# Performance work log

Hardware: AMD Instinct MI355X
Metric: run time of the kernel (lower is better)

## Reference

```python
import jax, jax.numpy as jnp
import numpy as np


def setup_inputs() -> dict:
    key = jax.random.key(0)
    k1, k2 = jax.random.split(key)
    B, S, D, E = 4, 4096, 2048, 64
    x = jax.random.normal(k1, (B, S, D), dtype=jnp.float32)
    # nn.Linear default init ~ U(-1/sqrt(D), 1/sqrt(D)); scale down for stability
    w_gate = jax.random.normal(k2, (E, D), dtype=jnp.float32) * (1.0 / np.sqrt(D))
    expert_bias = jnp.zeros((E,), dtype=jnp.float32)
    return {"x": x, "w_gate": w_gate, "expert_bias": expert_bias}


def reference(x, w_gate, expert_bias):
    # gate_logits: [B, S, E]
    gate_logits = jnp.einsum('bsd,ed->bse', x, w_gate)
    gate_weights = jax.nn.sigmoid(gate_logits)
    biased_logits = gate_logits + expert_bias
    k = 8  # num_experts_per_tok
    _, topk_indices = jax.lax.top_k(biased_logits, k)  # [B, S, k]
    topk_weights = jnp.take_along_axis(gate_weights, topk_indices, axis=-1)
    topk_weights = topk_weights / jnp.sum(topk_weights, axis=-1, keepdims=True)
    return topk_weights, topk_indices
```

## Files before the change

kernel.cpp:

```cpp
#include <hip/hip_runtime.h>
#include <math.h>

#define BLOCK 256
#define RB 32
#define BD 64
#define NE 64
#define DDIM 2048
#define TOPK 8
#define NCHUNK (DDIM / BD)

typedef float __attribute__((ext_vector_type(4))) f32x4;

__global__ __launch_bounds__(BLOCK, 2) void gate_kernel(
    const float* __restrict__ x,
    const float* __restrict__ w,
    const float* __restrict__ bias,
    float* __restrict__ out_w,
    float* __restrict__ out_i)
{
    __shared__ float xs[2][RB * BD];
    __shared__ float ws[2][NE * BD];

    const int t    = threadIdx.x;
    const int lane = t & 63;
    const int wid  = t >> 6;
    const int kc   = lane & 15;
    const int kh   = lane >> 4;
    const int row0 = blockIdx.x * RB;

    float acc[8][16];
#pragma unroll
    for (int r = 0; r < 8; ++r)
#pragma unroll
        for (int j = 0; j < 16; ++j) acc[r][j] = 0.f;

#define ISSUE(c_, xb_, wb_)                                                    \
    {                                                                          \
        const int d0_ = (c_) * BD;                                             \
        _Pragma("unroll")                                                      \
        for (int i = 0; i < 2; ++i) {                                          \
            int s  = wid * 2 + i;                                              \
            int f  = s * 256 + lane * 4;                                       \
            int xr = f >> 6, xc = f & 63;                                      \
            __builtin_amdgcn_global_load_lds(                                  \
                (const __attribute__((address_space(1))) unsigned int*)        \
                    (x + (size_t)(row0 + xr) * DDIM + d0_ + xc),               \
                (__attribute__((address_space(3))) unsigned int*)((xb_) + s * 256), \
                16, 0, 0);                                                     \
        }                                                                      \
        _Pragma("unroll")                                                      \
        for (int i = 0; i < 4; ++i) {                                          \
            int s  = wid * 4 + i;                                              \
            int f  = s * 256 + lane * 4;                                       \
            int wr = f >> 6, wc = f & 63;                                      \
            __builtin_amdgcn_global_load_lds(                                  \
                (const __attribute__((address_space(1))) unsigned int*)        \
                    (w + (size_t)wr * DDIM + d0_ + wc),                        \
                (__attribute__((address_space(3))) unsigned int*)((wb_) + s * 256), \
                16, 0, 0);                                                     \
        }                                                                      \
    }

    ISSUE(0, xs[0], ws[0]);

    for (int c = 0; c < NCHUNK; ++c) {
        __syncthreads();

        const float* xsb = xs[c & 1];
        const float* wsb = ws[c & 1];
        if (c + 1 < NCHUNK) ISSUE(c + 1, xs[(c + 1) & 1], ws[(c + 1) & 1]);

        f32x4 xv[8];
#pragma unroll
        for (int r = 0; r < 8; ++r)
            xv[r] = *(const f32x4*)&xsb[(wid * 8 + r) * BD + kc * 4];

#pragma unroll
        for (int j = 0; j < 16; ++j) {
            f32x4 wj = *(const f32x4*)&wsb[(kh * 16 + j) * BD + kc * 4];
#pragma unroll
            for (int r = 0; r < 8; ++r) {
                acc[r][j] += xv[r].x * wj.x;
                acc[r][j] += xv[r].y * wj.y;
                acc[r][j] += xv[r].z * wj.z;
                acc[r][j] += xv[r].w * wj.w;
            }
        }
    }

    const float bias_l = bias[lane];

#pragma unroll
    for (int r = 0; r < 8; ++r) {
        const int gr = row0 + wid * 8 + r;

        float v[16];
#pragma unroll
        for (int j = 0; j < 16; ++j) v[j] = acc[r][j];
#pragma unroll
        for (int o = 8; o; o >>= 1) {
            bool hi = (kc & o) != 0;
#pragma unroll
            for (int j = 0; j < o; ++j) {
                float send = hi ? v[j] : v[j + o];
                float keep = hi ? v[j + o] : v[j];
                v[j] = keep + __shfl_xor(send, o);
            }
        }
        float raw = v[0];
        float sig = 1.f / (1.f + expf(-raw));
        float vv  = raw + bias_l;

        float wsum = 0.f, myw = 0.f;
        int   myidx = 0;
#pragma unroll
        for (int k = 0; k < TOPK; ++k) {
            float m = vv;
#pragma unroll
            for (int off = 32; off; off >>= 1)
                m = fmaxf(m, __shfl_xor(m, off));
            unsigned long long b = __ballot(vv == m);
            int idx = (int)__builtin_ctzll(b);
            float wk = __shfl(sig, idx);
            wsum += wk;
            if (lane == k)  { myw = wk; myidx = idx; }
            if (lane == idx) vv = -INFINITY;
        }
        if (lane < TOPK) {
            out_w[(size_t)gr * TOPK + lane] = myw / wsum;
            out_i[(size_t)gr * TOPK + lane] = (float)myidx;
        }
    }
}

extern "C" void kernel_launch(void* const* d_in, const int* in_sizes, int n_in,
                              void* d_out, int out_size, void* d_ws, size_t ws_size,
                              hipStream_t stream) {
    const float* x    = (const float*)d_in[0];
    const float* w    = (const float*)d_in[1];
    const float* bias = (const float*)d_in[2];
    const int NR = in_sizes[0] / DDIM;
    float* out   = (float*)d_out;
    float* out_w = out;
    float* out_i = out + (size_t)NR * TOPK;

    dim3 grid(NR / RB), block(BLOCK);
    hipLaunchKernelGGL(gate_kernel, grid, block, 0, stream,
                       x, w, bias, out_w, out_i);
}
```

Baseline: 80.06 us.

## Load x tiles directly into registers with double buffering instead of LDS

The x rows are no longer staged through shared memory. Each thread loads its own f32x4 slices of x straight from global memory into two ping-pong register sets, prefetching the next chunk while computing the current one. Only the gate weights still go through the LDS double buffer. This cuts LDS traffic and footprint for x, at the cost of more live registers (16 extra vectors) and loads that are less coalesced, since each wave reads 8 rows with 16 lanes per row. This could raise register pressure under the launch bound of 2.

Measured after the change: 207.4 us. 2.59x slower.

```diff
diff --git a/kernel.cpp b/kernel.cpp
--- a/kernel.cpp
+++ b/kernel.cpp
@@ -18,7 +18,6 @@
     float* __restrict__ out_w,
     float* __restrict__ out_i)
 {
-    __shared__ float xs[2][RB * BD];
     __shared__ float ws[2][NE * BD];
 
     const int t    = threadIdx.x;
@@ -34,20 +33,9 @@
 #pragma unroll
         for (int j = 0; j < 16; ++j) acc[r][j] = 0.f;
 
-#define ISSUE(c_, xb_, wb_)                                                    \
+#define ISSUE_W(c_, wb_)                                                       \
     {                                                                          \
         const int d0_ = (c_) * BD;                                             \
-        _Pragma("unroll")                                                      \
-        for (int i = 0; i < 2; ++i) {                                          \
-            int s  = wid * 2 + i;                                              \
-            int f  = s * 256 + lane * 4;                                       \
-            int xr = f >> 6, xc = f & 63;                                      \
-            __builtin_amdgcn_global_load_lds(                                  \
-                (const __attribute__((address_space(1))) unsigned int*)        \
-                    (x + (size_t)(row0 + xr) * DDIM + d0_ + xc),               \
-                (__attribute__((address_space(3))) unsigned int*)((xb_) + s * 256), \
-                16, 0, 0);                                                     \
-        }                                                                      \
         _Pragma("unroll")                                                      \
         for (int i = 0; i < 4; ++i) {                                          \
             int s  = wid * 4 + i;                                              \
@@ -61,31 +49,42 @@
         }                                                                      \
     }
 
-    ISSUE(0, xs[0], ws[0]);
+    const float* xb = x + (size_t)(row0 + wid * 8) * DDIM + kc * 4;
+#define LOAD_X(dst_, c_)                                                       \
+    {                                                                          \
+        _Pragma("unroll")                                                      \
+        for (int r = 0; r < 8; ++r)                                            \
+            dst_[r] = *(const f32x4*)(xb + (size_t)r * DDIM + (c_) * BD);      \
+    }
 
-    for (int c = 0; c < NCHUNK; ++c) {
-        __syncthreads();
+    f32x4 xA[8], xB[8];
+    LOAD_X(xA, 0);
+    ISSUE_W(0, ws[0]);
 
-        const float* xsb = xs[c & 1];
-        const float* wsb = ws[c & 1];
-        if (c + 1 < NCHUNK) ISSUE(c + 1, xs[(c + 1) & 1], ws[(c + 1) & 1]);
+#define CHUNK_BODY(XCUR, XNXT, c_)                                             \
+    {                                                                          \
+        __syncthreads();     \
+        if ((c_) + 1 < NCHUNK) {                                               \
+            ISSUE_W((c_) + 1, ws[((c_) + 1) & 1]);  \
+            LOAD_X(XNXT, (c_) + 1);                  \
+        }                                                                      \
+        const float* wsb = ws[(c_) & 1];                                       \
+        _Pragma("unroll")                                                      \
+        for (int j = 0; j < 16; ++j) {                                         \
+            f32x4 wj = *(const f32x4*)&wsb[(kh * 16 + j) * BD + kc * 4];       \
+            _Pragma("unroll")                                                  \
+            for (int r = 0; r < 8; ++r) {                                      \
+                acc[r][j] += XCUR[r].x * wj.x;                                 \
+                acc[r][j] += XCUR[r].y * wj.y;                                 \
+                acc[r][j] += XCUR[r].z * wj.z;                                 \
+                acc[r][j] += XCUR[r].w * wj.w;                                 \
+            }                                                                  \
+        }                                                                      \
+    }
 
-        f32x4 xv[8];
-#pragma unroll
-        for (int r = 0; r < 8; ++r)
-            xv[r] = *(const f32x4*)&xsb[(wid * 8 + r) * BD + kc * 4];
-
-#pragma unroll
-        for (int j = 0; j < 16; ++j) {
-            f32x4 wj = *(const f32x4*)&wsb[(kh * 16 + j) * BD + kc * 4];
-#pragma unroll
-            for (int r = 0; r < 8; ++r) {
-                acc[r][j] += xv[r].x * wj.x;
-                acc[r][j] += xv[r].y * wj.y;
-                acc[r][j] += xv[r].z * wj.z;
-                acc[r][j] += xv[r].w * wj.w;
-            }
-        }
+    for (int c = 0; c < NCHUNK; c += 2) {
+        CHUNK_BODY(xA, xB, c);
+        CHUNK_BODY(xB, xA, c + 1);
     }
 
     const float bias_l = bias[lane];
```

## Halve row tile, load x straight to registers, split experts across waves

Applied to the files above, without the earlier changes.

Shrinks the row tile from 32 to 16 and asks for 4 blocks per CU instead of 2. The x tile is no longer staged through LDS: each thread loads its x fragment from global memory directly into registers, prefetching the next chunk after the compute. Waves now split experts into two halves, which halves the accumulator registers, and per-row logits go through a shared buffer before the top-k stage. This aims at higher occupancy and less LDS traffic, at the cost of uncoalesced-ish direct global loads for x and an extra barrier plus LDS round trip.

After: 130.0 us. +62.4%, slower.

```diff
diff --git a/kernel.cpp b/kernel.cpp
--- a/kernel.cpp
+++ b/kernel.cpp
@@ -2,7 +2,7 @@
 #include <math.h>
 
 #define BLOCK 256
-#define RB 32
+#define RB 16
 #define BD 64
 #define NE 64
 #define DDIM 2048
@@ -11,43 +11,34 @@
 
 typedef float __attribute__((ext_vector_type(4))) f32x4;
 
-__global__ __launch_bounds__(BLOCK, 2) void gate_kernel(
+__global__ __launch_bounds__(BLOCK, 4) void gate_kernel(
     const float* __restrict__ x,
     const float* __restrict__ w,
     const float* __restrict__ bias,
     float* __restrict__ out_w,
     float* __restrict__ out_i)
 {
-    __shared__ float xs[2][RB * BD];
     __shared__ float ws[2][NE * BD];
+    __shared__ float logits[RB][NE + 1];
 
     const int t    = threadIdx.x;
     const int lane = t & 63;
     const int wid  = t >> 6;
+    const int rw   = wid & 1;
+    const int eh   = wid >> 1;
     const int kc   = lane & 15;
-    const int kh   = lane >> 4;
+    const int kh   = (lane >> 4) & 3;
     const int row0 = blockIdx.x * RB;
 
-    float acc[8][16];
+    float acc[8][8];
 #pragma unroll
     for (int r = 0; r < 8; ++r)
 #pragma unroll
-        for (int j = 0; j < 16; ++j) acc[r][j] = 0.f;
+        for (int j = 0; j < 8; ++j) acc[r][j] = 0.f;
 
-#define ISSUE(c_, xb_, wb_)                                                    \
+#define ISSUE_W(c_, wb_)                                                       \
     {                                                                          \
         const int d0_ = (c_) * BD;                                             \
-        _Pragma("unroll")                                                      \
-        for (int i = 0; i < 2; ++i) {                                          \
-            int s  = wid * 2 + i;                                              \
-            int f  = s * 256 + lane * 4;                                       \
-            int xr = f >> 6, xc = f & 63;                                      \
-            __builtin_amdgcn_global_load_lds(                                  \
-                (const __attribute__((address_space(1))) unsigned int*)        \
-                    (x + (size_t)(row0 + xr) * DDIM + d0_ + xc),               \
-                (__attribute__((address_space(3))) unsigned int*)((xb_) + s * 256), \
-                16, 0, 0);                                                     \
-        }                                                                      \
         _Pragma("unroll")                                                      \
         for (int i = 0; i < 4; ++i) {                                          \
             int s  = wid * 4 + i;                                              \
@@ -61,23 +52,29 @@
         }                                                                      \
     }
 
-    ISSUE(0, xs[0], ws[0]);
+    const float* xb = x + (size_t)(row0 + rw * 8) * DDIM + kc * 4;
+    f32x4 xv[8];
+#define LOAD_XV(c_)                                                            \
+    {                                                                          \
+        _Pragma("unroll")                                                      \
+        for (int r = 0; r < 8; ++r)                                            \
+            xv[r] = *(const f32x4*)(xb + (size_t)r * DDIM + (c_) * BD);        \
+    }
+
+    ISSUE_W(0, ws[0]);
+    LOAD_XV(0);
+
+    const int wofs = (eh * 32 + kh * 8) * BD + kc * 4;
 
     for (int c = 0; c < NCHUNK; ++c) {
         __syncthreads();
 
-        const float* xsb = xs[c & 1];
+        if (c + 1 < NCHUNK) ISSUE_W(c + 1, ws[(c + 1) & 1]);
+
         const float* wsb = ws[c & 1];
-        if (c + 1 < NCHUNK) ISSUE(c + 1, xs[(c + 1) & 1], ws[(c + 1) & 1]);
-
-        f32x4 xv[8];
 #pragma unroll
-        for (int r = 0; r < 8; ++r)
-            xv[r] = *(const f32x4*)&xsb[(wid * 8 + r) * BD + kc * 4];
-
-#pragma unroll
-        for (int j = 0; j < 16; ++j) {
-            f32x4 wj = *(const f32x4*)&wsb[(kh * 16 + j) * BD + kc * 4];
+        for (int j = 0; j < 8; ++j) {
+            f32x4 wj = *(const f32x4*)&wsb[wofs + j * BD];
 #pragma unroll
             for (int r = 0; r < 8; ++r) {
                 acc[r][j] += xv[r].x * wj.x;
@@ -86,19 +83,20 @@
                 acc[r][j] += xv[r].w * wj.w;
             }
         }
+
+        __builtin_amdgcn_sched_barrier(0);
+        if (c + 1 < NCHUNK) LOAD_XV(c + 1);
     }
-
-    const float bias_l = bias[lane];
 
 #pragma unroll
     for (int r = 0; r < 8; ++r) {
-        const int gr = row0 + wid * 8 + r;
-
-        float v[16];
+        float v[8];
 #pragma unroll
-        for (int j = 0; j < 16; ++j) v[j] = acc[r][j];
+        for (int j = 0; j < 8; ++j) v[j] = acc[r][j];
 #pragma unroll
-        for (int o = 8; o; o >>= 1) {
+        for (int j = 0; j < 8; ++j) v[j] += __shfl_xor(v[j], 8);
+#pragma unroll
+        for (int o = 4; o; o >>= 1) {
             bool hi = (kc & o) != 0;
 #pragma unroll
             for (int j = 0; j < o; ++j) {
@@ -107,7 +105,16 @@
                 v[j] = keep + __shfl_xor(send, o);
             }
         }
-        float raw = v[0];
+        if (kc < 8)
+            logits[rw * 8 + r][eh * 32 + kh * 8 + kc] = v[0];
+    }
+    __syncthreads();
+
+    const float bias_l = bias[lane];
+    for (int rr = 0; rr < 4; ++rr) {
+        const int r  = wid * 4 + rr;
+        const int gr = row0 + r;
+        float raw = logits[r][lane];
         float sig = 1.f / (1.f + expf(-raw));
         float vv  = raw + bias_l;
 
```

## Replace LDS double-buffered staging with direct global-to-register loads

Applied to the files above, without the earlier changes.

Removes the shared-memory staging of x and w tiles (async global_load_lds with double buffering and per-chunk barriers) and has each thread load its x rows and w rows directly from global memory into registers every chunk. This drops LDS traffic and __syncthreads, but it also drops the explicit prefetch overlap. The four warps now each fetch the w tile separately, relying on L1/L2 to absorb the duplication. Holding 24 extra float4 values per thread raises register pressure alongside the 128 accumulators, which may limit occupancy or cause spills.

After: 144.7 us. +80.8%, slower.

```diff
diff --git a/kernel.cpp b/kernel.cpp
--- a/kernel.cpp
+++ b/kernel.cpp
@@ -18,9 +18,6 @@
     float* __restrict__ out_w,
     float* __restrict__ out_i)
 {
-    __shared__ float xs[2][RB * BD];
-    __shared__ float ws[2][NE * BD];
-
     const int t    = threadIdx.x;
     const int lane = t & 63;
     const int wid  = t >> 6;
@@ -34,56 +31,30 @@
 #pragma unroll
         for (int j = 0; j < 16; ++j) acc[r][j] = 0.f;
 
-#define ISSUE(c_, xb_, wb_)                                                    \
-    {                                                                          \
-        const int d0_ = (c_) * BD;                                             \
-        _Pragma("unroll")                                                      \
-        for (int i = 0; i < 2; ++i) {                                          \
-            int s  = wid * 2 + i;                                              \
-            int f  = s * 256 + lane * 4;                                       \
-            int xr = f >> 6, xc = f & 63;                                      \
-            __builtin_amdgcn_global_load_lds(                                  \
-                (const __attribute__((address_space(1))) unsigned int*)        \
-                    (x + (size_t)(row0 + xr) * DDIM + d0_ + xc),               \
-                (__attribute__((address_space(3))) unsigned int*)((xb_) + s * 256), \
-                16, 0, 0);                                                     \
-        }                                                                      \
-        _Pragma("unroll")                                                      \
-        for (int i = 0; i < 4; ++i) {                                          \
-            int s  = wid * 4 + i;                                              \
-            int f  = s * 256 + lane * 4;                                       \
-            int wr = f >> 6, wc = f & 63;                                      \
-            __builtin_amdgcn_global_load_lds(                                  \
-                (const __attribute__((address_space(1))) unsigned int*)        \
-                    (w + (size_t)wr * DDIM + d0_ + wc),                        \
-                (__attribute__((address_space(3))) unsigned int*)((wb_) + s * 256), \
-                16, 0, 0);                                                     \
-        }                                                                      \
-    }
-
-    ISSUE(0, xs[0], ws[0]);
+    const float* xb = x + (size_t)(row0 + wid * 8) * DDIM + kc * 4;
+    const float* wb = w + (size_t)(kh * 16) * DDIM + kc * 4;
 
     for (int c = 0; c < NCHUNK; ++c) {
-        __syncthreads();
-
-        const float* xsb = xs[c & 1];
-        const float* wsb = ws[c & 1];
-        if (c + 1 < NCHUNK) ISSUE(c + 1, xs[(c + 1) & 1], ws[(c + 1) & 1]);
+        const int d0 = c * BD;
 
         f32x4 xv[8];
 #pragma unroll
         for (int r = 0; r < 8; ++r)
-            xv[r] = *(const f32x4*)&xsb[(wid * 8 + r) * BD + kc * 4];
+            xv[r] = *(const f32x4*)(xb + (size_t)r * DDIM + d0);
+
+        f32x4 wv[16];
+#pragma unroll
+        for (int j = 0; j < 16; ++j)
+            wv[j] = *(const f32x4*)(wb + (size_t)j * DDIM + d0);
 
 #pragma unroll
         for (int j = 0; j < 16; ++j) {
-            f32x4 wj = *(const f32x4*)&wsb[(kh * 16 + j) * BD + kc * 4];
 #pragma unroll
             for (int r = 0; r < 8; ++r) {
-                acc[r][j] += xv[r].x * wj.x;
-                acc[r][j] += xv[r].y * wj.y;
-                acc[r][j] += xv[r].z * wj.z;
-                acc[r][j] += xv[r].w * wj.w;
+                acc[r][j] += xv[r].x * wv[j].x;
+                acc[r][j] += xv[r].y * wv[j].y;
+                acc[r][j] += xv[r].z * wv[j].z;
+                acc[r][j] += xv[r].w * wv[j].w;
             }
         }
     }
```
